# Performance work log

Hardware: AMD Instinct MI355X
Metric: run time of the kernel (lower is better)

## Reference

```python
import jax, jax.numpy as jnp
import numpy as np

B, N, F, G, M, E = 8, 512, 64, 64, 4, 4
L0 = 256          # NodeEmbedding hidden width (layers[0])
ALPHA = 0.5
EPS = 1e-5        # BatchNorm eps (training mode, batch stats)
NEG = -9e15       # masked-out logit value from the torch code


def _glorot(key, shape):
    # matches repo's glorot(): U(-s, s), s = sqrt(6/(fan_in+fan_out)) on last two dims
    s = float(np.sqrt(6.0 / (shape[-2] + shape[-1])))
    return jax.random.uniform(key, shape, minval=-s, maxval=s, dtype=jnp.float32)


def _xavier(key, shape, gain=1.0):
    s = gain * float(np.sqrt(6.0 / (shape[-2] + shape[-1])))
    return jax.random.uniform(key, shape, minval=-s, maxval=s, dtype=jnp.float32)


def setup_inputs() -> dict:
    key = jax.random.key(0)
    ks = jax.random.split(key, 8)
    A = jax.random.randint(ks[0], (B, E, N, N), 0, 2).astype(jnp.int32)  # dense 0/1 adjacency per edge cat
    X = jax.random.normal(ks[1], (B, N, F), dtype=jnp.float32)
    Ws = _glorot(ks[2], (E, M * F, G))                     # per-edge-cat stacked multi-head proj
    a1 = _xavier(ks[3], (E, M * G, 1), gain=1.414)
    a2 = _xavier(ks[4], (E, M * G, 1), gain=1.414)
    W_emb1 = _xavier(ks[5], (F, M * E * G))                # Embedding1: Linear(M*E*G -> F, no bias)
    W2a = _xavier(ks[6], (L0, F))                          # NodeEmbedding linear0: F -> L0
    W2b = _xavier(ks[7], (F, L0))                          # NodeEmbedding linear1: L0 -> F
    return {"A": A, "X": X, "Ws": Ws, "a1": a1, "a2": a2,
            "W_emb1": W_emb1, "W2a": W2a, "W2b": W2b, "mini_batch": 1}


def _bn(x):
    # BatchNorm1d in training mode, weight=1, bias=0, biased variance
    mu = x.mean(axis=0)
    var = x.var(axis=0)
    return (x - mu) / jnp.sqrt(var + EPS)


def reference(A, X, Ws, a1, a2, W_emb1, W2a, W2b, mini_batch):
    Wsr = Ws.reshape(E, M, F, G)        # per edge-cat, per head projection
    a1r = a1.reshape(E, M, G)
    a2r = a2.reshape(E, M, G)

    # Wh[b,e,m,n,g] = X[b] @ Ws[e] head m
    Wh = jnp.einsum('bnf,emfg->bemng', X, Wsr)
    s1 = jnp.einsum('bemng,emg->bemn', Wh, a1r)
    s2 = jnp.einsum('bemng,emg->bemn', Wh, a2r)
    logits = jax.nn.leaky_relu(s1[..., :, None] + s2[..., None, :])  # [B,E,M,N,N]
    logits = jnp.where(A[:, :, None, :, :] > 0, logits, NEG)
    att = jax.nn.softmax(logits, axis=-1)                            # softmax over neighbors (dim=1 of NxN)
    H = jax.nn.elu(jnp.einsum('bemij,bemjg->bemig', att, Wh))        # [B,E,M,N,G]

    # layout matches torch reshapes: feature index = m*(E*G) + e*G + g
    H = H.transpose(0, 3, 2, 1, 4).reshape(B * N, M * E * G)
    H = H @ W_emb1.T                                                 # Embedding1
    Xf = X.reshape(B * N, F)
    H = _bn((1.0 - ALPHA) * H + ALPHA * Xf)                          # BN1 with residual mix

    # NodeEmbedding: Linear -> BN -> ELU -> Linear
    Z = jax.nn.elu(_bn(H @ W2a.T)) @ W2b.T
    Z = _bn(H + Z)                                                   # BN2 residual
    return Z.reshape(B, N, F)
```

## Files before the change

kernel.cpp:

```cpp
#include <hip/hip_runtime.h>
#include <math.h>

#define B_   8
#define N_   512
#define F_   64
#define G_   64
#define M_   4
#define E_   4
#define MEG  1024

typedef __attribute__((ext_vector_type(8))) __bf16 bf16x8;
typedef __attribute__((ext_vector_type(4))) float f32x4;
typedef unsigned short ush;

static __device__ __forceinline__ ush bfu(float x) { __bf16 h = (__bf16)x; return __builtin_bit_cast(ush, h); }
static __device__ __forceinline__ bf16x8 asbf(int4 v) { return __builtin_bit_cast(bf16x8, v); }

__global__ void __launch_bounds__(256) kprep(const float* __restrict__ X, const float* __restrict__ Ws,
                                             const float* __restrict__ a1, const float* __restrict__ a2,
                                             const float* __restrict__ W_emb1, const float* __restrict__ W2a,
                                             const float* __restrict__ W2b,
                                             ush* __restrict__ Xb, ush* __restrict__ WsT, ush* __restrict__ cpack,
                                             ush* __restrict__ W1b, ush* __restrict__ W2ab, ush* __restrict__ W2bb) {
  int idx = blockIdx.x * 256 + threadIdx.x;
  if (idx < 65536) {
    float4 v = ((const float4*)X)[idx];
    ushort4 o; o.x = bfu(v.x); o.y = bfu(v.y); o.z = bfu(v.z); o.w = bfu(v.w);
    ((ushort4*)Xb)[idx] = o;
  } else if (idx < 131072) {
    int j = idx - 65536; int em = j >> 12, g = (j >> 6) & 63, f = j & 63;
    WsT[j] = bfu(Ws[em * 4096 + f * 64 + g]);
  } else if (idx < 132096) {
    int j = idx - 131072; int em = j >> 6, f = j & 63;
    const float* wp = Ws + em * 4096 + f * 64;
    const float* p1 = a1 + em * 64; const float* p2 = a2 + em * 64;
    float c1 = 0.f, c2 = 0.f;
    for (int g = 0; g < 64; ++g) { float w = wp[g]; c1 = fmaf(w, p1[g], c1); c2 = fmaf(w, p2[g], c2); }
    cpack[em * 1024 + f] = bfu(c1);
    cpack[em * 1024 + 64 + f] = bfu(c2);
    for (int r = 2; r < 16; ++r) cpack[em * 1024 + r * 64 + f] = 0;
  } else if (idx < 148480) {
    int j = idx - 132096;
    float4 v = ((const float4*)W_emb1)[j];
    ushort4 o; o.x = bfu(v.x); o.y = bfu(v.y); o.z = bfu(v.z); o.w = bfu(v.w);
    ((ushort4*)W1b)[j] = o;
  } else if (idx < 152576) {
    int j = idx - 148480;
    float4 v = ((const float4*)W2a)[j];
    ushort4 o; o.x = bfu(v.x); o.y = bfu(v.y); o.z = bfu(v.z); o.w = bfu(v.w);
    ((ushort4*)W2ab)[j] = o;
  } else if (idx < 156672) {
    int j = idx - 152576;
    float4 v = ((const float4*)W2b)[j];
    ushort4 o; o.x = bfu(v.x); o.y = bfu(v.y); o.z = bfu(v.z); o.w = bfu(v.w);
    ((ushort4*)W2bb)[j] = o;
  }
}

__global__ void __launch_bounds__(256) k1_wh(const ush* __restrict__ Xb, const ush* __restrict__ WsT,
                                             const ush* __restrict__ cpack, const int* __restrict__ A,
                                             ush* __restrict__ WhF, float* __restrict__ s1,
                                             float2* __restrict__ E2, unsigned* __restrict__ Amask) {
  const int tid = threadIdx.x, lane = tid & 63, w = tid >> 6, c = lane & 15, grp = lane >> 4;
  const int blk = blockIdx.x, nt = blk & 7, em = (blk >> 3) & 15, b = blk >> 7;
  const int n0 = nt * 64, bem = b * 16 + em;

  {
    const int w2 = blk * 256 + tid;
    const int* ap = A + (w2 >> 4) * 32 * 16 + (w2 & 15) * 32;
    unsigned bits = 0;
#pragma unroll
    for (int kq = 0; kq < 32; kq += 4) {
      int4 v = *(const int4*)(ap + kq);
      bits |= (v.x > 0 ? 1u : 0u) << kq;
      bits |= (v.y > 0 ? 1u : 0u) << (kq + 1);
      bits |= (v.z > 0 ? 1u : 0u) << (kq + 2);
      bits |= (v.w > 0 ? 1u : 0u) << (kq + 3);
    }
    Amask[w2] = bits;
  }

  f32x4 acc[4] = {};
  const ush* wsrow = WsT + em * 4096 + (w * 16 + c) * 64;
#pragma unroll
  for (int kk = 0; kk < 2; ++kk) {
    bf16x8 af = asbf(*(const int4*)(wsrow + kk * 32 + grp * 8));
#pragma unroll
    for (int t = 0; t < 4; ++t) {
      bf16x8 bv = asbf(*(const int4*)(Xb + (b * 512 + n0 + t * 16 + c) * 64 + kk * 32 + grp * 8));
      acc[t] = __builtin_amdgcn_mfma_f32_16x16x32_bf16(af, bv, acc[t], 0, 0, 0);
    }
  }
  ush* wout = WhF + bem * 32768;
#pragma unroll
  for (int t = 0; t < 4; ++t) {
    const int s  = nt * 2 + (t >> 1);
    const int gp = (t & 1) * 2 + (c >> 3);
    const int ii = c & 7;
#pragma unroll
    for (int r = 0; r < 4; ++r) {
      const int lane2 = gp * 16 + grp * 4 + r;
      wout[s * 2048 + w * 512 + lane2 * 8 + ii] = bfu(acc[t][r]);
    }
  }
  if (w == 0) {
    f32x4 sacc[4] = {};
    const ush* crow = cpack + em * 1024 + c * 64;
#pragma unroll
    for (int kk = 0; kk < 2; ++kk) {
      bf16x8 af = asbf(*(const int4*)(crow + kk * 32 + grp * 8));
#pragma unroll
      for (int t = 0; t < 4; ++t) {
        bf16x8 bv = asbf(*(const int4*)(Xb + (b * 512 + n0 + t * 16 + c) * 64 + kk * 32 + grp * 8));
        sacc[t] = __builtin_amdgcn_mfma_f32_16x16x32_bf16(af, bv, sacc[t], 0, 0, 0);
      }
    }
    if (grp == 0) {
#pragma unroll
      for (int t = 0; t < 4; ++t) {
        float s2v = sacc[t][1];
        s1[bem * 512 + n0 + t * 16 + c] = sacc[t][0];
        E2[bem * 512 + n0 + t * 16 + c] = make_float2(__expf(s2v), __expf(0.01f * s2v));
      }
    }
  }
}

__global__ void __launch_bounds__(256) k2_attn(const unsigned* __restrict__ Amask,
                                               const ush* __restrict__ WhF,
                                               const float* __restrict__ s1,
                                               const float2* __restrict__ E2,
                                               ush* __restrict__ Hb) {
  const int tid = threadIdx.x, lane = tid & 63, m = tid >> 6;
  const int grp = lane >> 4, col = lane & 15;
  const int blk = blockIdx.x;
  const int xcd = blk & 7, kk2 = blk >> 3;
  const int be = xcd * 4 + (kk2 >> 5), itile = kk2 & 31;
  const int b = be >> 2, e = be & 3;
  const int i0 = itile * 16;
  const int bem = be * 4 + m;

  __shared__ unsigned maskw[16][17];
  __shared__ float2 e2l[4][512];

  {
    const int row = tid >> 4, c = tid & 15;
    maskw[row][c] = Amask[(be * 512 + i0 + row) * 16 + c];
  }
  {
    const float2* e2g = E2 + bem * 512;
#pragma unroll
    for (int t = 0; t < 8; ++t) e2l[m][t * 64 + lane] = e2g[t * 64 + lane];
  }
  __syncthreads();

  const float s1row = s1[bem * N_ + i0 + col];
  const float e1p = __expf(s1row);
  const float e1n = __expf(0.01f * s1row);
  const float te  = __expf(-s1row);

  const ush* whb = WhF + bem * 32768 + lane * 8;
  f32x4 acc0 = {0.f, 0.f, 0.f, 0.f};
  f32x4 acc1 = acc0, acc2 = acc0, acc3 = acc0, accs = acc0;
  bf16x8 ones;
#pragma unroll
  for (int i = 0; i < 8; ++i) ones[i] = (__bf16)1.0f;

  int4 c0 = *(const int4*)(whb + 0);
  int4 c1 = *(const int4*)(whb + 512);
  int4 c2 = *(const int4*)(whb + 1024);
  int4 c3 = *(const int4*)(whb + 1536);
#pragma unroll 4
  for (int s = 0; s < 16; ++s) {
    const int noff = ((s + 1) & 15) * 2048;
    int4 n0 = *(const int4*)(whb + noff);
    int4 n1 = *(const int4*)(whb + noff + 512);
    int4 n2 = *(const int4*)(whb + noff + 1024);
    int4 n3 = *(const int4*)(whb + noff + 1536);

    unsigned mb = maskw[col][s] >> (grp * 8);
    const float2* ep = &e2l[m][s * 32 + grp * 8];
    bf16x8 af;
#pragma unroll
    for (int i = 0; i < 8; ++i) {
      float2 q = ep[i];
      float p = (q.x > te) ? q.x * e1p : q.y * e1n;
      p = ((mb >> i) & 1u) ? p : 0.f;
      af[i] = (__bf16)p;
    }
    accs = __builtin_amdgcn_mfma_f32_16x16x32_bf16(af, ones, accs, 0, 0, 0);
    acc0 = __builtin_amdgcn_mfma_f32_16x16x32_bf16(af, asbf(c0), acc0, 0, 0, 0);
    acc1 = __builtin_amdgcn_mfma_f32_16x16x32_bf16(af, asbf(c1), acc1, 0, 0, 0);
    acc2 = __builtin_amdgcn_mfma_f32_16x16x32_bf16(af, asbf(c2), acc2, 0, 0, 0);
    acc3 = __builtin_amdgcn_mfma_f32_16x16x32_bf16(af, asbf(c3), acc3, 0, 0, 0);
    c0 = n0; c1 = n1; c2 = n2; c3 = n3;
  }

  ush* op = Hb + (b * N_ + i0 + grp * 4) * MEG + m * 256 + e * 64 + col;
#pragma unroll
  for (int r = 0; r < 4; ++r) {
    float sv2 = accs[r];
    float inv = sv2 > 0.f ? 1.f / sv2 : 0.f;
    float v0 = acc0[r] * inv; v0 = v0 > 0.f ? v0 : expm1f(v0);
    float v1 = acc1[r] * inv; v1 = v1 > 0.f ? v1 : expm1f(v1);
    float v2 = acc2[r] * inv; v2 = v2 > 0.f ? v2 : expm1f(v2);
    float v3 = acc3[r] * inv; v3 = v3 > 0.f ? v3 : expm1f(v3);
    op[r * MEG + 0]  = bfu(v0);
    op[r * MEG + 16] = bfu(v1);
    op[r * MEG + 32] = bfu(v2);
    op[r * MEG + 48] = bfu(v3);
  }
}

__global__ void __launch_bounds__(256) k3_emb(const ush* __restrict__ Hb, const ush* __restrict__ W1b,
                                              const float* __restrict__ X, float* __restrict__ R,
                                              float* __restrict__ P2R) {
  const int tid = threadIdx.x, lane = tid & 63, w = tid >> 6, c = lane & 15, grp = lane >> 4;
  const int r0 = blockIdx.x * 16;
  const ush* ha = Hb + (r0 + c) * 1024 + grp * 8;
  const ush* wb = W1b + (w * 16 + c) * 1024 + grp * 8;
  f32x4 accA = {}, accB = {};
#pragma unroll 8
  for (int kk = 0; kk < 32; kk += 2) {
    accA = __builtin_amdgcn_mfma_f32_16x16x32_bf16(asbf(*(const int4*)(ha + kk * 32)),
                                                   asbf(*(const int4*)(wb + kk * 32)), accA, 0, 0, 0);
    accB = __builtin_amdgcn_mfma_f32_16x16x32_bf16(asbf(*(const int4*)(ha + kk * 32 + 32)),
                                                   asbf(*(const int4*)(wb + kk * 32 + 32)), accB, 0, 0, 0);
  }
  f32x4 acc = accA + accB;
  const int col = w * 16 + c;
  float s = 0.f, q = 0.f;
#pragma unroll
  for (int r = 0; r < 4; ++r) {
    int row = r0 + grp * 4 + r;
    float v = 0.5f * acc[r] + 0.5f * X[row * 64 + col];
    R[row * 64 + col] = v;
    s += v; q = fmaf(v, v, q);
  }
  s += __shfl_xor(s, 16); s += __shfl_xor(s, 32);
  q += __shfl_xor(q, 16); q += __shfl_xor(q, 32);
  if (grp == 0) { P2R[blockIdx.x * 128 + col] = s; P2R[blockIdx.x * 128 + 64 + col] = q; }
}

__global__ void __launch_bounds__(256) k4_node1(const float* __restrict__ R, const float* __restrict__ P2R,
                                                const ush* __restrict__ W2ab,
                                                float* __restrict__ T, float* __restrict__ P2T) {
  const int tid = threadIdx.x, lane = tid & 63, w = tid >> 6, c = lane & 15, grp = lane >> 4;
  const int r0 = blockIdx.x * 16, cb = w * 64;
  __shared__ float muR[64], rsR[64];
  if (tid < 128) {
    const int cc = tid & 63;
    float a = 0.f;
    for (int bk = 0; bk < 256; ++bk) a += P2R[bk * 128 + tid];
    if (tid < 64) muR[cc] = a * (1.f / 4096.f); else rsR[cc] = a;
  }
  __syncthreads();
  if (tid < 64) {
    float m = muR[tid];
    float v = rsR[tid] * (1.f / 4096.f) - m * m;
    rsR[tid] = rsqrtf(v + 1e-5f);
  }
  __syncthreads();

  f32x4 acc[4] = {};
#pragma unroll
  for (int kk = 0; kk < 2; ++kk) {
    const float* rp = R + (r0 + c) * 64 + kk * 32 + grp * 8;
    float4 v0 = *(const float4*)rp;
    float4 v1 = *(const float4*)(rp + 4);
    float vv[8] = {v0.x, v0.y, v0.z, v0.w, v1.x, v1.y, v1.z, v1.w};
    bf16x8 af;
#pragma unroll
    for (int i = 0; i < 8; ++i) {
      int f = kk * 32 + grp * 8 + i;
      af[i] = (__bf16)((vv[i] - muR[f]) * rsR[f]);
    }
#pragma unroll
    for (int ct = 0; ct < 4; ++ct) {
      bf16x8 bv = asbf(*(const int4*)(W2ab + (cb + ct * 16 + c) * 64 + kk * 32 + grp * 8));
      acc[ct] = __builtin_amdgcn_mfma_f32_16x16x32_bf16(af, bv, acc[ct], 0, 0, 0);
    }
  }
#pragma unroll
  for (int ct = 0; ct < 4; ++ct) {
    const int col = cb + ct * 16 + c;
    float s = 0.f, q = 0.f;
#pragma unroll
    for (int r = 0; r < 4; ++r) {
      float v = acc[ct][r];
      T[(r0 + grp * 4 + r) * 256 + col] = v;
      s += v; q = fmaf(v, v, q);
    }
    s += __shfl_xor(s, 16); s += __shfl_xor(s, 32);
    q += __shfl_xor(q, 16); q += __shfl_xor(q, 32);
    if (grp == 0) { P2T[blockIdx.x * 512 + col] = s; P2T[blockIdx.x * 512 + 256 + col] = q; }
  }
}

__global__ void __launch_bounds__(256) k5_node2(const float* __restrict__ T, const float* __restrict__ P2T,
                                                const ush* __restrict__ W2bb,
                                                const float* __restrict__ R, const float* __restrict__ P2R,
                                                float* __restrict__ S, float* __restrict__ P2S) {
  const int tid = threadIdx.x, lane = tid & 63, w = tid >> 6, c = lane & 15, grp = lane >> 4;
  const int r0 = blockIdx.x * 16;
  __shared__ float muT[256], rsT[256], muR[64], rsR[64];
  {
    float s = 0.f, q = 0.f;
    for (int bk = 0; bk < 256; ++bk) {
      s += P2T[bk * 512 + tid];
      q += P2T[bk * 512 + 256 + tid];
    }
    float m = s * (1.f / 4096.f);
    float v = q * (1.f / 4096.f) - m * m;
    muT[tid] = m; rsT[tid] = rsqrtf(v + 1e-5f);
  }
  if (tid < 128) {
    const int cc = tid & 63;
    float a = 0.f;
    for (int bk = 0; bk < 256; ++bk) a += P2R[bk * 128 + tid];
    if (tid < 64) muR[cc] = a * (1.f / 4096.f); else rsR[cc] = a;
  }
  __syncthreads();
  if (tid < 64) {
    float m = muR[tid];
    float v = rsR[tid] * (1.f / 4096.f) - m * m;
    rsR[tid] = rsqrtf(v + 1e-5f);
  }
  __syncthreads();

  f32x4 accA = {}, accB = {};
  const ush* wrow = W2bb + (w * 16 + c) * 256 + grp * 8;
  const float* trow = T + (r0 + c) * 256 + grp * 8;
#pragma unroll
  for (int kk = 0; kk < 8; ++kk) {
    float4 v0 = *(const float4*)(trow + kk * 32);
    float4 v1 = *(const float4*)(trow + kk * 32 + 4);
    float vv[8] = {v0.x, v0.y, v0.z, v0.w, v1.x, v1.y, v1.z, v1.w};
    bf16x8 af;
#pragma unroll
    for (int i = 0; i < 8; ++i) {
      int u = kk * 32 + grp * 8 + i;
      float t = (vv[i] - muT[u]) * rsT[u];
      t = t > 0.f ? t : expm1f(t);
      af[i] = (__bf16)t;
    }
    bf16x8 bv = asbf(*(const int4*)(wrow + kk * 32));
    if (kk & 1) accB = __builtin_amdgcn_mfma_f32_16x16x32_bf16(af, bv, accB, 0, 0, 0);
    else        accA = __builtin_amdgcn_mfma_f32_16x16x32_bf16(af, bv, accA, 0, 0, 0);
  }
  f32x4 acc = accA + accB;
  const int col = w * 16 + c;
  const float mu = muR[col], rsv = rsR[col];
  float s = 0.f, q = 0.f;
#pragma unroll
  for (int r = 0; r < 4; ++r) {
    int row = r0 + grp * 4 + r;
    float v = acc[r] + (R[row * 64 + col] - mu) * rsv;
    S[row * 64 + col] = v;
    s += v; q = fmaf(v, v, q);
  }
  s += __shfl_xor(s, 16); s += __shfl_xor(s, 32);
  q += __shfl_xor(q, 16); q += __shfl_xor(q, 32);
  if (grp == 0) { P2S[blockIdx.x * 128 + col] = s; P2S[blockIdx.x * 128 + 64 + col] = q; }
}

__global__ void __launch_bounds__(256) k6_bn(const float* __restrict__ S, const float* __restrict__ P2S,
                                             float* __restrict__ out) {
  const int tid = threadIdx.x;
  const int r0 = blockIdx.x * 16;
  __shared__ float muS[64], rsS[64];
  if (tid < 128) {
    const int cc = tid & 63;
    float a = 0.f;
    for (int bk = 0; bk < 256; ++bk) a += P2S[bk * 128 + tid];
    if (tid < 64) muS[cc] = a * (1.f / 4096.f); else rsS[cc] = a;
  }
  __syncthreads();
  if (tid < 64) {
    float m = muS[tid];
    float v = rsS[tid] * (1.f / 4096.f) - m * m;
    rsS[tid] = rsqrtf(v + 1e-5f);
  }
  __syncthreads();
  const int f0 = (tid * 4) & 63;
  float4 v = *(const float4*)(S + r0 * 64 + tid * 4);
  float4 o;
  o.x = (v.x - muS[f0 + 0]) * rsS[f0 + 0];
  o.y = (v.y - muS[f0 + 1]) * rsS[f0 + 1];
  o.z = (v.z - muS[f0 + 2]) * rsS[f0 + 2];
  o.w = (v.w - muS[f0 + 3]) * rsS[f0 + 3];
  *(float4*)(out + r0 * 64 + tid * 4) = o;
}

extern "C" void kernel_launch(void* const* d_in, const int* in_sizes, int n_in,
                              void* d_out, int out_size, void* d_ws, size_t ws_size,
                              hipStream_t stream) {
  const int*   A      = (const int*)d_in[0];
  const float* X      = (const float*)d_in[1];
  const float* Ws     = (const float*)d_in[2];
  const float* a1     = (const float*)d_in[3];
  const float* a2     = (const float*)d_in[4];
  const float* W_emb1 = (const float*)d_in[5];
  const float* W2a    = (const float*)d_in[6];
  const float* W2b    = (const float*)d_in[7];
  float* out = (float*)d_out;

  float* ws = (float*)d_ws;
  ush*   Hb    = (ush*)d_ws;
  ush*   WhF   = (ush*)(ws + 2097152);
  float* s1    = ws + 4194304;
  float2* E2   = (float2*)(ws + 4259840);
  ush*   Xb    = (ush*)(ws + 4390912);
  ush*   WsT   = (ush*)(ws + 4521984);
  ush*   cpack = (ush*)(ws + 4554752);
  ush*   W1b   = (ush*)(ws + 4562944);
  ush*   W2ab  = (ush*)(ws + 4595712);
  ush*   W2bb  = (ush*)(ws + 4603904);
  float* R     = ws + 4612096;
  float* T     = ws + 4874240;
  float* S     = ws + 5922816;
  float* P2R   = ws + 6184960;
  float* P2T   = ws + 6217728;
  float* P2S   = ws + 6348800;
  unsigned* Amask = (unsigned*)R;

  kprep<<<612, 256, 0, stream>>>(X, Ws, a1, a2, W_emb1, W2a, W2b, Xb, WsT, cpack, W1b, W2ab, W2bb);
  k1_wh<<<1024, 256, 0, stream>>>(Xb, WsT, cpack, A, WhF, s1, E2, Amask);
  k2_attn<<<1024, 256, 0, stream>>>(Amask, WhF, s1, E2, Hb);
  k3_emb<<<256, 256, 0, stream>>>(Hb, W1b, X, R, P2R);
  k4_node1<<<256, 256, 0, stream>>>(R, P2R, W2ab, T, P2T);
  k5_node2<<<256, 256, 0, stream>>>(T, P2T, W2bb, R, P2R, S, P2S);
  k6_bn<<<256, 256, 0, stream>>>(S, P2S, out);
}
```

Before: 97.10 us.

## Fold weight-prep kernel into consumers with in-kernel bf16 conversion via LDS staging

Measured after the change: 96.71 us. No clear change (-0.4%).

```diff
diff --git a/kernel.cpp b/kernel.cpp
--- a/kernel.cpp
+++ b/kernel.cpp
@@ -15,59 +15,30 @@
 
 static __device__ __forceinline__ ush bfu(float x) { __bf16 h = (__bf16)x; return __builtin_bit_cast(ush, h); }
 static __device__ __forceinline__ bf16x8 asbf(int4 v) { return __builtin_bit_cast(bf16x8, v); }
-
-__global__ void __launch_bounds__(256) kprep(const float* __restrict__ X, const float* __restrict__ Ws,
+static __device__ __forceinline__ bf16x8 cvt8(float4 a, float4 b) {
+  bf16x8 r;
+  r[0] = (__bf16)a.x; r[1] = (__bf16)a.y; r[2] = (__bf16)a.z; r[3] = (__bf16)a.w;
+  r[4] = (__bf16)b.x; r[5] = (__bf16)b.y; r[6] = (__bf16)b.z; r[7] = (__bf16)b.w;
+  return r;
+}
+
+__global__ void __launch_bounds__(256) k1_wh(const float* __restrict__ X, const float* __restrict__ Ws,
                                              const float* __restrict__ a1, const float* __restrict__ a2,
-                                             const float* __restrict__ W_emb1, const float* __restrict__ W2a,
-                                             const float* __restrict__ W2b,
-                                             ush* __restrict__ Xb, ush* __restrict__ WsT, ush* __restrict__ cpack,
-                                             ush* __restrict__ W1b, ush* __restrict__ W2ab, ush* __restrict__ W2bb) {
-  int idx = blockIdx.x * 256 + threadIdx.x;
-  if (idx < 65536) {
-    float4 v = ((const float4*)X)[idx];
-    ushort4 o; o.x = bfu(v.x); o.y = bfu(v.y); o.z = bfu(v.z); o.w = bfu(v.w);
-    ((ushort4*)Xb)[idx] = o;
-  } else if (idx < 131072) {
-    int j = idx - 65536; int em = j >> 12, g = (j >> 6) & 63, f = j & 63;
-    WsT[j] = bfu(Ws[em * 4096 + f * 64 + g]);
-  } else if (idx < 132096) {
-    int j = idx - 131072; int em = j >> 6, f = j & 63;
-    const float* wp = Ws + em * 4096 + f * 64;
-    const float* p1 = a1 + em * 64; const float* p2 = a2 + em * 64;
-    float c1 = 0.f, c2 = 0.f;
-    for (int g = 0; g < 64; ++g) { float w = wp[g]; c1 = fmaf(w, p1[g], c1); c2 = fmaf(w, p2[g], c2); }
-    cpack[em * 1024 + f] = bfu(c1);
-    cpack[em * 1024 + 64 + f] = bfu(c2);
-    for (int r = 2; r < 16; ++r) cpack[em * 1024 + r * 64 + f] = 0;
-  } else if (idx < 148480) {
-    int j = idx - 132096;
-    float4 v = ((const float4*)W_emb1)[j];
-    ushort4 o; o.x = bfu(v.x); o.y = bfu(v.y); o.z = bfu(v.z); o.w = bfu(v.w);
-    ((ushort4*)W1b)[j] = o;
-  } else if (idx < 152576) {
-    int j = idx - 148480;
-    float4 v = ((const float4*)W2a)[j];
-    ushort4 o; o.x = bfu(v.x); o.y = bfu(v.y); o.z = bfu(v.z); o.w = bfu(v.w);
-    ((ushort4*)W2ab)[j] = o;
-  } else if (idx < 156672) {
-    int j = idx - 152576;
-    float4 v = ((const float4*)W2b)[j];
-    ushort4 o; o.x = bfu(v.x); o.y = bfu(v.y); o.z = bfu(v.z); o.w = bfu(v.w);
-    ((ushort4*)W2bb)[j] = o;
-  }
-}
-
-__global__ void __launch_bounds__(256) k1_wh(const ush* __restrict__ Xb, const ush* __restrict__ WsT,
-                                             const ush* __restrict__ cpack, const int* __restrict__ A,
+                                             const int* __restrict__ A,
                                              ush* __restrict__ WhF, float* __restrict__ s1,
                                              float2* __restrict__ E2, unsigned* __restrict__ Amask) {
   const int tid = threadIdx.x, lane = tid & 63, w = tid >> 6, c = lane & 15, grp = lane >> 4;
   const int blk = blockIdx.x, nt = blk & 7, em = (blk >> 3) & 15, b = blk >> 7;
   const int n0 = nt * 64, bem = b * 16 + em;
 
+  __shared__ __align__(16) ush xl[2][4][64][8];
+  __shared__ __align__(16) ush wl[2][4][64][8];
+  __shared__ float c1b[64], c2b[64];
+  __shared__ __align__(16) ush st[4096];
+
   {
     const int w2 = blk * 256 + tid;
-    const int* ap = A + (w2 >> 4) * 32 * 16 + (w2 & 15) * 32;
+    const int* ap = A + (w2 >> 4) * 512 + (w2 & 15) * 32;
     unsigned bits = 0;
 #pragma unroll
     for (int kq = 0; kq < 32; kq += 4) {
@@ -80,38 +51,83 @@
     Amask[w2] = bits;
   }
 
+  {
+    const int row = tid >> 2, cg = tid & 3;
+    const int t = row >> 4, cc = row & 15;
+    const float* xp = X + (b * 512 + n0 + row) * 64 + cg * 16;
+#pragma unroll
+    for (int q4 = 0; q4 < 4; ++q4) {
+      float4 v = ((const float4*)xp)[q4];
+      float vals[4] = {v.x, v.y, v.z, v.w};
+#pragma unroll
+      for (int u = 0; u < 4; ++u) {
+        const int f = cg * 16 + q4 * 4 + u;
+        xl[f >> 5][t][((f >> 3) & 3) * 16 + cc][f & 7] = bfu(vals[u]);
+      }
+    }
+  }
+  {
+    const int f = tid >> 2, gq = tid & 3;
+    const int kk = f >> 5, gg = (f >> 3) & 3, ii = f & 7;
+    const float* wp = Ws + em * 4096 + f * 64 + gq * 16;
+    const float* p1 = a1 + em * 64 + gq * 16;
+    const float* p2 = a2 + em * 64 + gq * 16;
+    float d1 = 0.f, d2 = 0.f;
+#pragma unroll
+    for (int q4 = 0; q4 < 4; ++q4) {
+      float4 v  = ((const float4*)wp)[q4];
+      float4 va = ((const float4*)p1)[q4];
+      float4 vb = ((const float4*)p2)[q4];
+      float vals[4] = {v.x, v.y, v.z, v.w};
+      float aa[4] = {va.x, va.y, va.z, va.w};
+      float bb[4] = {vb.x, vb.y, vb.z, vb.w};
+#pragma unroll
+      for (int u = 0; u < 4; ++u) {
+        const int g = gq * 16 + q4 * 4 + u;
+        wl[kk][g >> 4][gg * 16 + (g & 15)][ii] = bfu(vals[u]);
+        d1 = fmaf(vals[u], aa[u], d1);
+        d2 = fmaf(vals[u], bb[u], d2);
+      }
+    }
+    d1 += __shfl_xor(d1, 1); d1 += __shfl_xor(d1, 2);
+    d2 += __shfl_xor(d2, 1); d2 += __shfl_xor(d2, 2);
+    if (gq == 0) { c1b[f] = d1; c2b[f] = d2; }
+  }
+  __syncthreads();
+
   f32x4 acc[4] = {};
-  const ush* wsrow = WsT + em * 4096 + (w * 16 + c) * 64;
 #pragma unroll
   for (int kk = 0; kk < 2; ++kk) {
-    bf16x8 af = asbf(*(const int4*)(wsrow + kk * 32 + grp * 8));
+    bf16x8 af = asbf(*(const int4*)&wl[kk][w][lane][0]);
 #pragma unroll
     for (int t = 0; t < 4; ++t) {
-      bf16x8 bv = asbf(*(const int4*)(Xb + (b * 512 + n0 + t * 16 + c) * 64 + kk * 32 + grp * 8));
+      bf16x8 bv = asbf(*(const int4*)&xl[kk][t][lane][0]);
       acc[t] = __builtin_amdgcn_mfma_f32_16x16x32_bf16(af, bv, acc[t], 0, 0, 0);
     }
   }
-  ush* wout = WhF + bem * 32768;
 #pragma unroll
   for (int t = 0; t < 4; ++t) {
-    const int s  = nt * 2 + (t >> 1);
+    const int sl = t >> 1;
     const int gp = (t & 1) * 2 + (c >> 3);
     const int ii = c & 7;
 #pragma unroll
-    for (int r = 0; r < 4; ++r) {
-      const int lane2 = gp * 16 + grp * 4 + r;
-      wout[s * 2048 + w * 512 + lane2 * 8 + ii] = bfu(acc[t][r]);
-    }
+    for (int r = 0; r < 4; ++r)
+      st[sl * 2048 + w * 512 + (gp * 16 + grp * 4 + r) * 8 + ii] = bfu(acc[t][r]);
   }
   if (w == 0) {
     f32x4 sacc[4] = {};
-    const ush* crow = cpack + em * 1024 + c * 64;
 #pragma unroll
     for (int kk = 0; kk < 2; ++kk) {
-      bf16x8 af = asbf(*(const int4*)(crow + kk * 32 + grp * 8));
+      bf16x8 af;
+#pragma unroll
+      for (int i = 0; i < 8; ++i) {
+        const int f = kk * 32 + grp * 8 + i;
+        float v = (c == 0) ? c1b[f] : (c == 1) ? c2b[f] : 0.f;
+        af[i] = (__bf16)v;
+      }
 #pragma unroll
       for (int t = 0; t < 4; ++t) {
-        bf16x8 bv = asbf(*(const int4*)(Xb + (b * 512 + n0 + t * 16 + c) * 64 + kk * 32 + grp * 8));
+        bf16x8 bv = asbf(*(const int4*)&xl[kk][t][lane][0]);
         sacc[t] = __builtin_amdgcn_mfma_f32_16x16x32_bf16(af, bv, sacc[t], 0, 0, 0);
       }
     }
@@ -123,6 +139,13 @@
         E2[bem * 512 + n0 + t * 16 + c] = make_float2(__expf(s2v), __expf(0.01f * s2v));
       }
     }
+  }
+  __syncthreads();
+  {
+    int4* dst = (int4*)(WhF + bem * 32768 + nt * 4096);
+    const int4* src = (const int4*)st;
+    dst[tid * 2]     = src[tid * 2];
+    dst[tid * 2 + 1] = src[tid * 2 + 1];
   }
 }
 
@@ -144,8 +167,8 @@
   __shared__ float2 e2l[4][512];
 
   {
-    const int row = tid >> 4, c = tid & 15;
-    maskw[row][c] = Amask[(be * 512 + i0 + row) * 16 + c];
+    const int row = tid >> 4, cc = tid & 15;
+    maskw[row][cc] = Amask[(be * 512 + i0 + row) * 16 + cc];
   }
   {
     const float2* e2g = E2 + bem * 512;
@@ -212,20 +235,20 @@
   }
 }
 
-__global__ void __launch_bounds__(256) k3_emb(const ush* __restrict__ Hb, const ush* __restrict__ W1b,
+__global__ void __launch_bounds__(256) k3_emb(const ush* __restrict__ Hb, const float* __restrict__ W_emb1,
                                               const float* __restrict__ X, float* __restrict__ R,
                                               float* __restrict__ P2R) {
   const int tid = threadIdx.x, lane = tid & 63, w = tid >> 6, c = lane & 15, grp = lane >> 4;
   const int r0 = blockIdx.x * 16;
   const ush* ha = Hb + (r0 + c) * 1024 + grp * 8;
-  const ush* wb = W1b + (w * 16 + c) * 1024 + grp * 8;
+  const float* wbf = W_emb1 + (w * 16 + c) * 1024 + grp * 8;
   f32x4 accA = {}, accB = {};
 #pragma unroll 8
   for (int kk = 0; kk < 32; kk += 2) {
-    accA = __builtin_amdgcn_mfma_f32_16x16x32_bf16(asbf(*(const int4*)(ha + kk * 32)),
-                                                   asbf(*(const int4*)(wb + kk * 32)), accA, 0, 0, 0);
-    accB = __builtin_amdgcn_mfma_f32_16x16x32_bf16(asbf(*(const int4*)(ha + kk * 32 + 32)),
-                                                   asbf(*(const int4*)(wb + kk * 32 + 32)), accB, 0, 0, 0);
+    bf16x8 w0 = cvt8(*(const float4*)(wbf + kk * 32),      *(const float4*)(wbf + kk * 32 + 4));
+    bf16x8 w1 = cvt8(*(const float4*)(wbf + kk * 32 + 32), *(const float4*)(wbf + kk * 32 + 36));
+    accA = __builtin_amdgcn_mfma_f32_16x16x32_bf16(asbf(*(const int4*)(ha + kk * 32)), w0, accA, 0, 0, 0);
+    accB = __builtin_amdgcn_mfma_f32_16x16x32_bf16(asbf(*(const int4*)(ha + kk * 32 + 32)), w1, accB, 0, 0, 0);
   }
   f32x4 acc = accA + accB;
   const int col = w * 16 + c;
@@ -243,7 +266,7 @@
 }
 
 __global__ void __launch_bounds__(256) k4_node1(const float* __restrict__ R, const float* __restrict__ P2R,
-                                                const ush* __restrict__ W2ab,
+                                                const float* __restrict__ W2a,
                                                 float* __restrict__ T, float* __restrict__ P2T) {
   const int tid = threadIdx.x, lane = tid & 63, w = tid >> 6, c = lane & 15, grp = lane >> 4;
   const int r0 = blockIdx.x * 16, cb = w * 64;
@@ -277,7 +300,8 @@
     }
 #pragma unroll
     for (int ct = 0; ct < 4; ++ct) {
-      bf16x8 bv = asbf(*(const int4*)(W2ab + (cb + ct * 16 + c) * 64 + kk * 32 + grp * 8));
+      const float* wp = W2a + (cb + ct * 16 + c) * 64 + kk * 32 + grp * 8;
+      bf16x8 bv = cvt8(*(const float4*)wp, *(const float4*)(wp + 4));
       acc[ct] = __builtin_amdgcn_mfma_f32_16x16x32_bf16(af, bv, acc[ct], 0, 0, 0);
     }
   }
@@ -298,7 +322,7 @@
 }
 
 __global__ void __launch_bounds__(256) k5_node2(const float* __restrict__ T, const float* __restrict__ P2T,
-                                                const ush* __restrict__ W2bb,
+                                                const float* __restrict__ W2b,
                                                 const float* __restrict__ R, const float* __restrict__ P2R,
                                                 float* __restrict__ S, float* __restrict__ P2S) {
   const int tid = threadIdx.x, lane = tid & 63, w = tid >> 6, c = lane & 15, grp = lane >> 4;
@@ -329,7 +353,7 @@
   __syncthreads();
 
   f32x4 accA = {}, accB = {};
-  const ush* wrow = W2bb + (w * 16 + c) * 256 + grp * 8;
+  const float* wrow = W2b + (w * 16 + c) * 256 + grp * 8;
   const float* trow = T + (r0 + c) * 256 + grp * 8;
 #pragma unroll
   for (int kk = 0; kk < 8; ++kk) {
@@ -344,7 +368,7 @@
       t = t > 0.f ? t : expm1f(t);
       af[i] = (__bf16)t;
     }
-    bf16x8 bv = asbf(*(const int4*)(wrow + kk * 32));
+    bf16x8 bv = cvt8(*(const float4*)(wrow + kk * 32), *(const float4*)(wrow + kk * 32 + 4));
     if (kk & 1) accB = __builtin_amdgcn_mfma_f32_16x16x32_bf16(af, bv, accB, 0, 0, 0);
     else        accA = __builtin_amdgcn_mfma_f32_16x16x32_bf16(af, bv, accA, 0, 0, 0);
   }
@@ -410,12 +434,6 @@
   ush*   WhF   = (ush*)(ws + 2097152);
   float* s1    = ws + 4194304;
   float2* E2   = (float2*)(ws + 4259840);
-  ush*   Xb    = (ush*)(ws + 4390912);
-  ush*   WsT   = (ush*)(ws + 4521984);
-  ush*   cpack = (ush*)(ws + 4554752);
-  ush*   W1b   = (ush*)(ws + 4562944);
-  ush*   W2ab  = (ush*)(ws + 4595712);
-  ush*   W2bb  = (ush*)(ws + 4603904);
   float* R     = ws + 4612096;
   float* T     = ws + 4874240;
   float* S     = ws + 5922816;
@@ -424,11 +442,10 @@
   float* P2S   = ws + 6348800;
   unsigned* Amask = (unsigned*)R;
 
-  kprep<<<612, 256, 0, stream>>>(X, Ws, a1, a2, W_emb1, W2a, W2b, Xb, WsT, cpack, W1b, W2ab, W2bb);
-  k1_wh<<<1024, 256, 0, stream>>>(Xb, WsT, cpack, A, WhF, s1, E2, Amask);
+  k1_wh<<<1024, 256, 0, stream>>>(X, Ws, a1, a2, A, WhF, s1, E2, Amask);
   k2_attn<<<1024, 256, 0, stream>>>(Amask, WhF, s1, E2, Hb);
-  k3_emb<<<256, 256, 0, stream>>>(Hb, W1b, X, R, P2R);
-  k4_node1<<<256, 256, 0, stream>>>(R, P2R, W2ab, T, P2T);
-  k5_node2<<<256, 256, 0, stream>>>(T, P2T, W2bb, R, P2R, S, P2S);
+  k3_emb<<<256, 256, 0, stream>>>(Hb, W_emb1, X, R, P2R);
+  k4_node1<<<256, 256, 0, stream>>>(R, P2R, W2a, T, P2T);
+  k5_node2<<<256, 256, 0, stream>>>(T, P2T, W2b, R, P2R, S, P2S);
   k6_bn<<<256, 256, 0, stream>>>(S, P2S, out);
 }
```
